# Kernel tuning notes

Measured on AMD Instinct MI355X. Metric: run time of the kernel, lower is better.

## Reference

```python
import jax, jax.numpy as jnp
import numpy as np

IN_DIM = 2048
HIDDEN = 5120
OUT_DIM = 1024
T = IN_DIM + HIDDEN + OUT_DIM  # total_units = 8192
NPROP = 8
N_PAIRS = T * (T - 1) // 2  # unique symmetric pair weights


def setup_inputs() -> dict:
    key = jax.random.key(0)
    k1, k2, k3 = jax.random.split(key, 3)
    return {
        "inputs": jax.random.normal(k1, (IN_DIM,), dtype=jnp.float32),
        "w_flat": jax.random.normal(k2, (N_PAIRS,), dtype=jnp.float32) * 0.01,
        "b": jax.random.normal(k3, (T,), dtype=jnp.float32) * 0.01,
    }


def _sym_matrix(w_flat):
    # Scatter the flat pair weights into the strict upper triangle, then
    # symmetrize. Diagonal stays zero: a node never attends to itself
    # (neighbor_nodes excludes states[node] in the original).
    iu, ju = jnp.triu_indices(T, k=1)
    M = jnp.zeros((T, T), dtype=w_flat.dtype).at[iu, ju].set(w_flat)
    return M + M.T


def reference(inputs, w_flat, b):
    M = _sym_matrix(w_flat)  # [T, T] symmetric, zero diagonal
    states = jnp.zeros((T,), dtype=inputs.dtype).at[:IN_DIM].set(inputs)

    def step(s, _):
        # new_state[n] = act(sum_{m != n} w_pair(n, m) * s[m] + b[n])
        s_new = jnp.tanh(M @ s + b)
        return s_new, None

    states, _ = jax.lax.scan(step, states, None, length=NPROP)
    return states[-OUT_DIM:]
```

## Files before the change

kernel.cpp:

```cpp
#include <hip/hip_runtime.h>
#include <hip/hip_fp16.h>


constexpr int T     = 8192;
constexpr int IN    = 2048;
constexpr int OUT   = 1024;
constexpr int NPROP = 8;

constexpr int TILE   = 128;
constexpr int NT     = T / TILE;
constexpr int NTILES = NT * (NT + 1) / 2;

__device__ __forceinline__ unsigned triidx(unsigned r, unsigned j) {
    return r * (unsigned)(T - 1) - ((r * (r - 1u)) >> 1) + j - r - 1u;
}

__device__ __forceinline__ int crow(int r) {
    int q = r >> 3, rem = r & 7;
    return r * T - 8 * (4 * q * (q - 1) + q * (rem + 1));
}
constexpr size_t W16_ALLOC = 33587200;

__host__ __device__ __forceinline__ unsigned rowstart(int b) {
    return (unsigned)(b * NT) - (unsigned)((b * (b - 1)) >> 1);
}

__device__ __forceinline__ void tile_decode(unsigned p, int& bi, int& bj) {
    const float A = (float)(2 * NT + 1);
    bi = (int)((A - sqrtf(A * A - 8.0f * (float)p)) * 0.5f);
    if (bi < 0) bi = 0;
    while (rowstart(bi + 1) <= p) ++bi;
    while (rowstart(bi) > p) --bi;
    bj = bi + (int)(p - rowstart(bi));
}

__device__ __forceinline__ uint4 pack8(const float* v) {
    uint4 pk;
    ushort* us = (ushort*)&pk;
    #pragma unroll
    for (int d = 0; d < 8; ++d) us[d] = __half_as_ushort(__float2half_rn(v[d]));
    return pk;
}

__global__ __launch_bounds__(256) void conv_kernel(const float* __restrict__ w,
                                                   __half* __restrict__ w16) {
    unsigned bid = blockIdx.x;
    int sweep = (int)(bid & 7u);
    int bi, bj; tile_decode(bid >> 3, bi, bj);
    int i0 = bi * TILE, j0 = bj * TILE;
    int t = threadIdx.x;
    int r  = i0 + sweep * 16 + (t >> 4);
    int jb = j0 + (t & 15) * 8;

    if (bi != bj || jb > r) {
        unsigned base = triidx((unsigned)r, (unsigned)jb);
        unsigned a0   = base & ~3u;
        int      sel  = (int)(base & 3u);
        float4 fA = *(const float4*)(w + a0);
        float4 fB = *(const float4*)(w + a0 + 4);
        float4 fC = *(const float4*)(w + a0 + 8);
        float v[8];
        if (sel == 0) {
            v[0]=fA.x; v[1]=fA.y; v[2]=fA.z; v[3]=fA.w;
            v[4]=fB.x; v[5]=fB.y; v[6]=fB.z; v[7]=fB.w;
        } else if (sel == 1) {
            v[0]=fA.y; v[1]=fA.z; v[2]=fA.w; v[3]=fB.x;
            v[4]=fB.y; v[5]=fB.z; v[6]=fB.w; v[7]=fC.x;
        } else if (sel == 2) {
            v[0]=fA.z; v[1]=fA.w; v[2]=fB.x; v[3]=fB.y;
            v[4]=fB.z; v[5]=fB.w; v[6]=fC.x; v[7]=fC.y;
        } else {
            v[0]=fA.w; v[1]=fB.x; v[2]=fB.y; v[3]=fB.z;
            v[4]=fB.w; v[5]=fC.x; v[6]=fC.y; v[7]=fC.z;
        }
        *(uint4*)(w16 + (crow(r) + jb)) = pack8(v);
    } else if (jb + 7 > r) {
        #pragma unroll
        for (int d = 0; d < 8; ++d) {
            int j = jb + d;
            if (j > r)
                w16[crow(r) + j] =
                    __float2half_rn(w[triidx((unsigned)r, (unsigned)j)]);
        }
    }
}

__global__ __launch_bounds__(256) void init_kernel(const float* __restrict__ in,
                                                   float* __restrict__ s,
                                                   float* __restrict__ y) {
    int n = blockIdx.x * 256 + threadIdx.x;
    if (n < T) { s[n] = (n < IN) ? in[n] : 0.0f; y[n] = 0.0f; }
}

__global__ __launch_bounds__(256) void sym_kernel(const __half* __restrict__ w16,
                                                  const float* __restrict__ s,
                                                  float* __restrict__ y, int mode) {
    __shared__ float sIl[TILE], sJl[TILE];
    __shared__ float colpart[4][TILE];

    int bi, bj; tile_decode(blockIdx.x, bi, bj);
    if (mode == 2 && bj < (T - OUT) / TILE) return;
    bool doRow = (mode == 0) ? true
               : (mode == 1) ? (bj < IN / TILE)
                             : (bi >= (T - OUT) / TILE);

    int i0 = bi * TILE, j0 = bj * TILE;
    int t = threadIdx.x;
    if (t < TILE) sIl[t] = s[i0 + t];
    else          sJl[t - TILE] = s[j0 + (t - TILE)];
    __syncthreads();

    int l = t & 63, wv = t >> 6;
    int g = l & 15, ro = l >> 4;
    int cbase = j0 + g * 8;

    float sjv[8];
    #pragma unroll
    for (int d = 0; d < 8; ++d) sjv[d] = sJl[g * 8 + d];
    float colacc[8] = {0.f, 0.f, 0.f, 0.f, 0.f, 0.f, 0.f, 0.f};

    #pragma unroll
    for (int k = 0; k < 8; ++k) {
        int rr = wv * 32 + k * 4 + ro;
        int r  = i0 + rr;
        uint4 wq = *(const uint4*)(w16 + (crow(r) + cbase));
        const __half2* h2 = (const __half2*)&wq;
        float2 f0 = __half22float2(h2[0]);
        float2 f1 = __half22float2(h2[1]);
        float2 f2 = __half22float2(h2[2]);
        float2 f3 = __half22float2(h2[3]);
        float wf[8] = {f0.x, f0.y, f1.x, f1.y, f2.x, f2.y, f3.x, f3.y};

        float si = sIl[rr];
        float rp = 0.0f;
        #pragma unroll
        for (int d = 0; d < 8; ++d) {
            float we = (cbase + d > r) ? wf[d] : 0.0f;
            colacc[d] = fmaf(we, si, colacc[d]);
            rp        = fmaf(we, sjv[d], rp);
        }
        if (doRow) {
            rp += __shfl_xor(rp, 1, 64);
            rp += __shfl_xor(rp, 2, 64);
            rp += __shfl_xor(rp, 4, 64);
            rp += __shfl_xor(rp, 8, 64);
            if (g == 0) atomicAdd(&y[r], rp);
        }
    }

    #pragma unroll
    for (int d = 0; d < 8; ++d) {
        colacc[d] += __shfl_xor(colacc[d], 16, 64);
        colacc[d] += __shfl_xor(colacc[d], 32, 64);
    }
    if (l < 16) {
        #pragma unroll
        for (int d = 0; d < 8; ++d) colpart[wv][g * 8 + d] = colacc[d];
    }
    __syncthreads();
    if (t < TILE) {
        float c = colpart[0][t] + colpart[1][t] + colpart[2][t] + colpart[3][t];
        atomicAdd(&y[j0 + t], c);
    }
}

__global__ __launch_bounds__(256) void act_kernel(const float* __restrict__ b,
                                                  float* __restrict__ s,
                                                  float* __restrict__ y) {
    int n = blockIdx.x * 256 + threadIdx.x;
    if (n < T) { s[n] = tanhf(y[n] + b[n]); y[n] = 0.0f; }
}

__global__ __launch_bounds__(256) void actout_kernel(const float* __restrict__ b,
                                                     const float* __restrict__ y,
                                                     float* __restrict__ o) {
    int n = blockIdx.x * 256 + threadIdx.x;
    if (n < OUT) o[n] = tanhf(y[T - OUT + n] + b[T - OUT + n]);
}

extern "C" void kernel_launch(void* const* d_in, const int* in_sizes, int n_in,
                              void* d_out, int out_size, void* d_ws, size_t ws_size,
                              hipStream_t stream) {
    const float* in = (const float*)d_in[0];
    const float* w  = (const float*)d_in[1];
    const float* b  = (const float*)d_in[2];
    float* out = (float*)d_out;

    __half* w16 = (__half*)d_ws;
    float*  s   = (float*)((char*)d_ws + W16_ALLOC * sizeof(__half));
    float*  y   = s + T;

    conv_kernel<<<NTILES * 8, 256, 0, stream>>>(w, w16);
    init_kernel<<<T / 256, 256, 0, stream>>>(in, s, y);

    sym_kernel<<<rowstart(IN / TILE), 256, 0, stream>>>(w16, s, y, 1);
    act_kernel<<<T / 256, 256, 0, stream>>>(b, s, y);
    for (int it = 1; it < NPROP - 1; ++it) {
        sym_kernel<<<NTILES, 256, 0, stream>>>(w16, s, y, 0);
        act_kernel<<<T / 256, 256, 0, stream>>>(b, s, y);
    }
    sym_kernel<<<NTILES, 256, 0, stream>>>(w16, s, y, 2);
    actout_kernel<<<OUT / 256, 256, 0, stream>>>(b, y, out);
}
```

Measured before the change: 185.1 us.

## Fuse tanh activation into sym kernel loads and restructure conversion by rows

The separate activation kernel is removed. Each sym_kernel block now computes tanh(y_prev + b) on the fly for the state slices it needs, reading from a per-iteration y buffer; all eight y buffers are zeroed once up front. The conversion kernel is rewritten to process one full triangular row per block, pairing row r with row T-1-r to balance the work and to read the flat weights contiguously. This saves seven kernel launches and their state round-trips, at the cost of redundant tanh evaluations and extra y workspace.

Result: faster. 171.4 us (-7.4%).

```diff
diff --git a/kernel.cpp b/kernel.cpp
--- a/kernel.cpp
+++ b/kernel.cpp
@@ -42,58 +42,61 @@
     return pk;
 }
 
+__device__ __forceinline__ void sel8(float4 fA, float4 fB, float4 fC, int sel,
+                                     float* v) {
+    if (sel == 0) {
+        v[0]=fA.x; v[1]=fA.y; v[2]=fA.z; v[3]=fA.w;
+        v[4]=fB.x; v[5]=fB.y; v[6]=fB.z; v[7]=fB.w;
+    } else if (sel == 1) {
+        v[0]=fA.y; v[1]=fA.z; v[2]=fA.w; v[3]=fB.x;
+        v[4]=fB.y; v[5]=fB.z; v[6]=fB.w; v[7]=fC.x;
+    } else if (sel == 2) {
+        v[0]=fA.z; v[1]=fA.w; v[2]=fB.x; v[3]=fB.y;
+        v[4]=fB.z; v[5]=fB.w; v[6]=fC.x; v[7]=fC.y;
+    } else {
+        v[0]=fA.w; v[1]=fB.x; v[2]=fB.y; v[3]=fB.z;
+        v[4]=fB.w; v[5]=fC.x; v[6]=fC.y; v[7]=fC.z;
+    }
+}
+
 __global__ __launch_bounds__(256) void conv_kernel(const float* __restrict__ w,
                                                    __half* __restrict__ w16) {
-    unsigned bid = blockIdx.x;
-    int sweep = (int)(bid & 7u);
-    int bi, bj; tile_decode(bid >> 3, bi, bj);
-    int i0 = bi * TILE, j0 = bj * TILE;
     int t = threadIdx.x;
-    int r  = i0 + sweep * 16 + (t >> 4);
-    int jb = j0 + (t & 15) * 8;
-
-    if (bi != bj || jb > r) {
-        unsigned base = triidx((unsigned)r, (unsigned)jb);
-        unsigned a0   = base & ~3u;
-        int      sel  = (int)(base & 3u);
-        float4 fA = *(const float4*)(w + a0);
-        float4 fB = *(const float4*)(w + a0 + 4);
-        float4 fC = *(const float4*)(w + a0 + 8);
-        float v[8];
-        if (sel == 0) {
-            v[0]=fA.x; v[1]=fA.y; v[2]=fA.z; v[3]=fA.w;
-            v[4]=fB.x; v[5]=fB.y; v[6]=fB.z; v[7]=fB.w;
-        } else if (sel == 1) {
-            v[0]=fA.y; v[1]=fA.z; v[2]=fA.w; v[3]=fB.x;
-            v[4]=fB.y; v[5]=fB.z; v[6]=fB.w; v[7]=fC.x;
-        } else if (sel == 2) {
-            v[0]=fA.z; v[1]=fA.w; v[2]=fB.x; v[3]=fB.y;
-            v[4]=fB.z; v[5]=fB.w; v[6]=fC.x; v[7]=fC.y;
-        } else {
-            v[0]=fA.w; v[1]=fB.x; v[2]=fB.y; v[3]=fB.z;
-            v[4]=fB.w; v[5]=fC.x; v[6]=fC.y; v[7]=fC.z;
+    #pragma unroll
+    for (int q = 0; q < 2; ++q) {
+        int r = (q == 0) ? (int)blockIdx.x : (T - 1 - (int)blockIdx.x);
+        int j1 = r + 1;
+        int jA = (j1 + 7) & ~7;
+        unsigned offr = triidx((unsigned)r, (unsigned)j1);
+        if (t < jA - j1)
+            w16[crow(r) + j1 + t] = __float2half_rn(w[offr + (unsigned)t]);
+        unsigned baseA = offr + (unsigned)(jA - j1);
+        int sel = (int)(baseA & 3u);
+        int cr = crow(r);
+        for (int j8 = jA + t * 8; j8 + 8 <= T; j8 += 8 * 256) {
+            unsigned a0 = (baseA + (unsigned)(j8 - jA)) & ~3u;
+            float4 fA = *(const float4*)(w + a0);
+            float4 fB = *(const float4*)(w + a0 + 4);
+            float4 fC = *(const float4*)(w + a0 + 8);
+            float v[8];
+            sel8(fA, fB, fC, sel, v);
+            *(uint4*)(w16 + (cr + j8)) = pack8(v);
         }
-        *(uint4*)(w16 + (crow(r) + jb)) = pack8(v);
-    } else if (jb + 7 > r) {
-        #pragma unroll
-        for (int d = 0; d < 8; ++d) {
-            int j = jb + d;
-            if (j > r)
-                w16[crow(r) + j] =
-                    __float2half_rn(w[triidx((unsigned)r, (unsigned)j)]);
-        }
     }
 }
 
 __global__ __launch_bounds__(256) void init_kernel(const float* __restrict__ in,
-                                                   float* __restrict__ s,
+                                                   float* __restrict__ s0,
                                                    float* __restrict__ y) {
     int n = blockIdx.x * 256 + threadIdx.x;
-    if (n < T) { s[n] = (n < IN) ? in[n] : 0.0f; y[n] = 0.0f; }
+    if (n < T) s0[n] = (n < IN) ? in[n] : 0.0f;
+    if (n < NPROP * T) y[n] = 0.0f;
 }
 
 __global__ __launch_bounds__(256) void sym_kernel(const __half* __restrict__ w16,
-                                                  const float* __restrict__ s,
+                                                  const float* __restrict__ sp,
+                                                  const float* __restrict__ yprev,
+                                                  const float* __restrict__ bv,
                                                   float* __restrict__ y, int mode) {
     __shared__ float sIl[TILE], sJl[TILE];
     __shared__ float colpart[4][TILE];
@@ -106,8 +109,12 @@
 
     int i0 = bi * TILE, j0 = bj * TILE;
     int t = threadIdx.x;
-    if (t < TILE) sIl[t] = s[i0 + t];
-    else          sJl[t - TILE] = s[j0 + (t - TILE)];
+    {
+        int idx = (t < TILE) ? (i0 + t) : (j0 + (t - TILE));
+        float sval = sp ? sp[idx] : tanhf(yprev[idx] + bv[idx]);
+        if (t < TILE) sIl[t] = sval;
+        else          sJl[t - TILE] = sval;
+    }
     __syncthreads();
 
     int l = t & 63, wv = t >> 6;
@@ -164,13 +171,6 @@
     }
 }
 
-__global__ __launch_bounds__(256) void act_kernel(const float* __restrict__ b,
-                                                  float* __restrict__ s,
-                                                  float* __restrict__ y) {
-    int n = blockIdx.x * 256 + threadIdx.x;
-    if (n < T) { s[n] = tanhf(y[n] + b[n]); y[n] = 0.0f; }
-}
-
 __global__ __launch_bounds__(256) void actout_kernel(const float* __restrict__ b,
                                                      const float* __restrict__ y,
                                                      float* __restrict__ o) {
@@ -187,18 +187,19 @@
     float* out = (float*)d_out;
 
     __half* w16 = (__half*)d_ws;
-    float*  s   = (float*)((char*)d_ws + W16_ALLOC * sizeof(__half));
-    float*  y   = s + T;
-
-    conv_kernel<<<NTILES * 8, 256, 0, stream>>>(w, w16);
-    init_kernel<<<T / 256, 256, 0, stream>>>(in, s, y);
-
-    sym_kernel<<<rowstart(IN / TILE), 256, 0, stream>>>(w16, s, y, 1);
-    act_kernel<<<T / 256, 256, 0, stream>>>(b, s, y);
+    float*  s0  = (float*)((char*)d_ws + W16_ALLOC * sizeof(__half));
+    float*  y   = s0 + T;
+
+    conv_kernel<<<T / 2, 256, 0, stream>>>(w, w16);
+    init_kernel<<<NPROP * T / 256, 256, 0, stream>>>(in, s0, y);
+
+    sym_kernel<<<rowstart(IN / TILE), 256, 0, stream>>>(w16, s0, nullptr, nullptr,
+                                                        y, 1);
     for (int it = 1; it < NPROP - 1; ++it) {
-        sym_kernel<<<NTILES, 256, 0, stream>>>(w16, s, y, 0);
-        act_kernel<<<T / 256, 256, 0, stream>>>(b, s, y);
-    }
-    sym_kernel<<<NTILES, 256, 0, stream>>>(w16, s, y, 2);
-    actout_kernel<<<OUT / 256, 256, 0, stream>>>(b, y, out);
-}
+        sym_kernel<<<NTILES, 256, 0, stream>>>(w16, nullptr, y + (it - 1) * T, b,
+                                               y + it * T, 0);
+    }
+    sym_kernel<<<NTILES, 256, 0, stream>>>(w16, nullptr, y + (NPROP - 2) * T, b,
+                                           y + (NPROP - 1) * T, 2);
+    actout_kernel<<<OUT / 256, 256, 0, stream>>>(b, y + (NPROP - 1) * T, out);
+}
```
